# Kernel tuning notes

Hardware: AMD Instinct MI355X
Metric: run time of the kernel (lower is better)

The kernel has to match this reference:

```python
import jax, jax.numpy as jnp
import numpy as np

N_PATHS = 100000
N_STEPS = 512          # number of Euler steps; paths have N_STEPS+1 time points
DT = 0.004             # step_size (~1/250, daily)
KAPPA = 1.0
THETA = 0.04
SIGMA = 0.2
RHO = -0.7
S0 = 100.0
V0 = 0.04


def setup_inputs() -> dict:
    key = jax.random.key(0)
    z = jax.random.normal(key, (N_PATHS, N_STEPS, 2), dtype=jnp.float32)
    return {"z": z}


def reference(z):
    # Euler-Maruyama simulation of the Heston SDE with full-truncation clamp:
    #   dS = S * sqrt(v) dW1
    #   dv = kappa*(theta - v) dt + sigma*sqrt(v) dW2,  corr(dW1,dW2)=rho
    sqdt = jnp.sqrt(jnp.float32(DT))
    c = jnp.sqrt(jnp.float32(1.0 - RHO * RHO))

    def step(carry, zt):
        s, v = carry                      # each [N]
        vp = jnp.maximum(v, 0.0)
        sv = jnp.sqrt(vp)
        dW1 = sqdt * zt[:, 0]
        dW2 = RHO * dW1 + c * sqdt * zt[:, 1]
        s_new = s + s * sv * dW1
        v_new = jnp.maximum(v + KAPPA * (THETA - vp) * DT + SIGMA * sv * dW2, 0.0)
        return (s_new, v_new), (s_new, v_new)

    s0 = jnp.full((N_PATHS,), S0, dtype=z.dtype)
    v0 = jnp.full((N_PATHS,), V0, dtype=z.dtype)
    _, (ss, vs) = jax.lax.scan(step, (s0, v0), jnp.transpose(z, (1, 0, 2)))

    prices = jnp.concatenate([s0[None], ss], axis=0).T      # [N, T+1]
    variances = jnp.concatenate([v0[None], vs], axis=0).T   # [N, T+1]

    # variance-swap price: cumsum of variance * dt + analytic remaining leg L
    tau = jnp.linspace(N_STEPS * DT, 0.0, N_STEPS + 1).astype(z.dtype)  # [T+1]
    L = (variances - THETA) / KAPPA * (1.0 - jnp.exp(-KAPPA * tau)) + THETA * tau
    varswap = jnp.cumsum(variances, axis=1) * DT + L        # [N, T+1]

    # [N, T+1, 3] = (price, variance, varswap price)
    return jnp.stack([prices, variances, varswap], axis=-1)
```

## Files before the change

kernel.cpp:

```cpp
#include <hip/hip_runtime.h>
#include <hip/hip_fp16.h>


#define N_PATHS 100000
#define N_STEPS 512
#define TROW    1539
#define PPB     48
#define BT      128
#define SUB     16
#define NSUB    32
#define U32ROW  770
#define DTc     0.004f
#define EDT     1.0040080107f

typedef float  f32x4  __attribute__((ext_vector_type(4)));
typedef __fp16 fp16x2 __attribute__((ext_vector_type(2)));

__device__ __forceinline__ unsigned pk2(float a, float b) {
    union { fp16x2 h; unsigned u; } cv;
    cv.h = __builtin_amdgcn_cvt_pkrtz(a, b);
    return cv.u;
}
__device__ __forceinline__ float exlo(unsigned w) {
    return __half2float(__ushort_as_half((unsigned short)(w & 0xFFFFu)));
}
__device__ __forceinline__ float exhi(unsigned w) {
    return __half2float(__ushort_as_half((unsigned short)(w >> 16)));
}

__global__ __launch_bounds__(BT)
void heston_kernel(const float* __restrict__ z, float* __restrict__ out) {
    __shared__ unsigned L32[PPB * U32ROW];

    const int tid = threadIdx.x;
    const int p0  = blockIdx.x * PPB;
    const int lim = (N_PATHS - p0 < PPB) ? (N_PATHS - p0) : PPB;

    if (tid < 64) {
        const int  lp  = tid;
        const bool act = (lp < PPB) && (p0 + lp < N_PATHS);
        const int  pc  = (p0 + lp < N_PATHS) ? (p0 + lp) : (N_PATHS - 1);
        const char* zp = (const char*)z + (size_t)pc * 4096;

        f32x4 fA[8], fB[8], fC[8];
        #pragma unroll
        for (int j = 0; j < 8; ++j) fA[j] = *(const f32x4*)(zp + 16 * j);
        #pragma unroll
        for (int j = 0; j < 8; ++j) fB[j] = *(const f32x4*)(zp + 128 + 16 * j);

        float s = 100.0f, v = 0.04f, acc = 0.04f, tau = 2.048f, e = expf(-2.048f);
        float sP = 0.f, vP = 0.f, vsP = 0.f;

        auto doSub = [&](int sc, f32x4 (&cur)[8], f32x4 (&pre)[8]) {
            if (sc + 2 < NSUB) {
                const char* zc = zp + (size_t)(sc + 2) * 128;
                #pragma unroll
                for (int j = 0; j < 8; ++j) pre[j] = *(const f32x4*)(zc + 16 * j);
            }
            const int ub = lp * U32ROW + sc * 24;
            #pragma unroll
            for (int dt = 0; dt < SUB; ++dt) {
                const f32x4 q  = cur[dt >> 1];
                const float z0 = (dt & 1) ? q.z : q.x;
                const float z1 = (dt & 1) ? q.w : q.y;

                const float vp  = fmaxf(v, 0.0f);
                const float sv  = __builtin_amdgcn_sqrtf(vp);
                const float dW1 = 0.06324555320f * z0;
                const float dW2 = fmaf(-0.7f, dW1, 0.04516636050f * z1);
                s = fmaf(s * sv, dW1, s);
                v = fmaxf(fmaf(0.2f * sv, dW2, fmaf(0.04f - vp, DTc, v)), 0.0f);
                acc += v;
                tau -= DTc;
                e *= EDT;
                const float vs = fmaf(acc, DTc, fmaf(0.04f, tau, (v - 0.04f) * (1.0f - e)));

                if (dt & 1) {
                    if (act) {
                        const int d = ub + 3 * (dt >> 1);
                        L32[d + 0] = pk2(sP, vP);
                        L32[d + 1] = pk2(vsP, s);
                        L32[d + 2] = pk2(v, vs);
                    }
                } else { sP = s; vP = v; vsP = vs; }
            }
        };

        for (int g = 0; g < 30; g += 3) {
            doSub(g + 0, fA, fC);
            doSub(g + 1, fB, fA);
            doSub(g + 2, fC, fB);
        }
        doSub(30, fA, fC);
        doSub(31, fB, fA);
    }

    __syncthreads();

    const int wv = tid >> 6;
    const int j  = tid & 63;

    for (int r = wv; r < lim; r += 2) {
        const size_t R0 = (size_t)(p0 + r) * TROW;
        float* gr = out + R0;
        const int hb = r * U32ROW;

        if (j < 3) gr[j] = (j == 0) ? 100.0f : ((j == 1) ? 0.04f : 0.08208f);

        const int lead = (int)((0u - (unsigned)((R0 + 3) & 3u)) & 3u);
        const int ng   = (1536 - lead) >> 2;
        const int tl   = (1536 - lead) & 3;

        if (j < lead) {
            const unsigned w = L32[hb + (j >> 1)];
            gr[3 + j] = (j & 1) ? exhi(w) : exlo(w);
        }
        if (j < tl) {
            const int idx = lead + 4 * ng + j;
            const unsigned w = L32[hb + (idx >> 1)];
            gr[3 + idx] = (idx & 1) ? exhi(w) : exlo(w);
        }

        const int sh = (lead & 1) * 16;
        float* gbase = gr + 3 + lead;
        #pragma unroll
        for (int k = 0; k < 6; ++k) {
            const int g = j + 64 * k;
            if (g < ng) {
                const int idx = lead + 4 * g;
                const int w0  = hb + (idx >> 1);
                const unsigned W0 = L32[w0];
                const unsigned W1 = L32[w0 + 1];
                const unsigned W2 = L32[w0 + 2];
                const unsigned lo = __builtin_amdgcn_alignbit(W1, W0, sh);
                const unsigned hi = __builtin_amdgcn_alignbit(W2, W1, sh);
                f32x4 o;
                o.x = exlo(lo); o.y = exhi(lo);
                o.z = exlo(hi); o.w = exhi(hi);
                *(f32x4*)(gbase + 4 * g) = o;
            }
        }
    }
}

extern "C" void kernel_launch(void* const* d_in, const int* in_sizes, int n_in,
                              void* d_out, int out_size, void* d_ws, size_t ws_size,
                              hipStream_t stream) {
    const float* z = (const float*)d_in[0];
    float* out = (float*)d_out;
    const int nblocks = (N_PATHS + PPB - 1) / PPB;
    heston_kernel<<<nblocks, BT, 0, stream>>>(z, out);
}
```

Baseline: 356.2 us.

## Make blocks persistent and double-buffer LDS so simulation overlaps output writes

Turns the kernel into a persistent grid of 256 blocks, each handling 17 tiles of 24 paths. Wave 0 simulates tile t into one half of a double-buffered LDS area while waves 1 and 2 expand and write tile t-1 from the other half to global memory. The goal is to hide the serial simulation latency behind the output stores instead of running the two phases back to back in each block. The trade-offs are fewer paths per simulating wave (24 of 64 lanes active), a per-tile barrier, and only 256 blocks to fill the GPU.

Result: slower. 473.8 us (+33.0%).

```diff
diff --git a/kernel.cpp b/kernel.cpp
--- a/kernel.cpp
+++ b/kernel.cpp
@@ -5,11 +5,13 @@
 #define N_PATHS 100000
 #define N_STEPS 512
 #define TROW    1539
-#define PPB     48
-#define BT      128
+#define PPB     24
+#define TTILES  17
+#define BT      192
 #define SUB     16
 #define NSUB    32
 #define U32ROW  770
+#define BUFU    (PPB * U32ROW)
 #define DTc     0.004f
 #define EDT     1.0040080107f
 
@@ -30,17 +32,20 @@
 
 __global__ __launch_bounds__(BT)
 void heston_kernel(const float* __restrict__ z, float* __restrict__ out) {
-    __shared__ unsigned L32[PPB * U32ROW];
+    __shared__ unsigned L32[2 * BUFU];
 
     const int tid = threadIdx.x;
-    const int p0  = blockIdx.x * PPB;
-    const int lim = (N_PATHS - p0 < PPB) ? (N_PATHS - p0) : PPB;
+    const int wv  = tid >> 6;
+    const int ln  = tid & 63;
+    const size_t pbase0 = (size_t)blockIdx.x * (PPB * TTILES);
 
-    if (tid < 64) {
-        const int  lp  = tid;
-        const bool act = (lp < PPB) && (p0 + lp < N_PATHS);
-        const int  pc  = (p0 + lp < N_PATHS) ? (p0 + lp) : (N_PATHS - 1);
-        const char* zp = (const char*)z + (size_t)pc * 4096;
+    auto simTile = [&](int t) {
+        const size_t pb = pbase0 + (size_t)t * PPB;
+        if (pb >= N_PATHS) return;
+        unsigned* buf = &L32[(t & 1) * BUFU];
+        const bool act = (ln < PPB) && (pb + ln < N_PATHS);
+        const size_t pc = (pb + ln < N_PATHS) ? (pb + ln) : (N_PATHS - 1);
+        const char* zp = (const char*)z + pc * 4096;
 
         f32x4 fA[8], fB[8], fC[8];
         #pragma unroll
@@ -57,7 +62,7 @@
                 #pragma unroll
                 for (int j = 0; j < 8; ++j) pre[j] = *(const f32x4*)(zc + 16 * j);
             }
-            const int ub = lp * U32ROW + sc * 24;
+            const int ub = ln * U32ROW + sc * 24;
             #pragma unroll
             for (int dt = 0; dt < SUB; ++dt) {
                 const f32x4 q  = cur[dt >> 1];
@@ -78,9 +83,9 @@
                 if (dt & 1) {
                     if (act) {
                         const int d = ub + 3 * (dt >> 1);
-                        L32[d + 0] = pk2(sP, vP);
-                        L32[d + 1] = pk2(vsP, s);
-                        L32[d + 2] = pk2(v, vs);
+                        buf[d + 0] = pk2(sP, vP);
+                        buf[d + 1] = pk2(vsP, s);
+                        buf[d + 2] = pk2(v, vs);
                     }
                 } else { sP = s; vP = v; vsP = vs; }
             }
@@ -93,54 +98,66 @@
         }
         doSub(30, fA, fC);
         doSub(31, fB, fA);
-    }
+    };
 
-    __syncthreads();
+    auto expTile = [&](int t) {
+        const size_t pb = pbase0 + (size_t)t * PPB;
+        if (pb >= N_PATHS) return;
+        const int lim = (int)((N_PATHS - pb < PPB) ? (N_PATHS - pb) : PPB);
+        const unsigned* buf = &L32[(t & 1) * BUFU];
+        const int j = ln;
 
-    const int wv = tid >> 6;
-    const int j  = tid & 63;
+        for (int rr = 0; rr < 12; ++rr) {
+            const int r = (wv - 1) * 12 + rr;
+            if (r >= lim) break;
+            const size_t R0 = (pb + r) * (size_t)TROW;
+            float* gr = out + R0;
+            const int hb = r * U32ROW;
 
-    for (int r = wv; r < lim; r += 2) {
-        const size_t R0 = (size_t)(p0 + r) * TROW;
-        float* gr = out + R0;
-        const int hb = r * U32ROW;
+            if (j < 3) gr[j] = (j == 0) ? 100.0f : ((j == 1) ? 0.04f : 0.08208f);
 
-        if (j < 3) gr[j] = (j == 0) ? 100.0f : ((j == 1) ? 0.04f : 0.08208f);
+            const int lead = (int)((0u - (unsigned)((R0 + 3) & 3u)) & 3u);
+            const int ng   = (1536 - lead) >> 2;
+            const int tl   = (1536 - lead) & 3;
 
-        const int lead = (int)((0u - (unsigned)((R0 + 3) & 3u)) & 3u);
-        const int ng   = (1536 - lead) >> 2;
-        const int tl   = (1536 - lead) & 3;
+            if (j < lead) {
+                const unsigned w = buf[hb + (j >> 1)];
+                gr[3 + j] = (j & 1) ? exhi(w) : exlo(w);
+            }
+            if (j < tl) {
+                const int idx = lead + 4 * ng + j;
+                const unsigned w = buf[hb + (idx >> 1)];
+                gr[3 + idx] = (idx & 1) ? exhi(w) : exlo(w);
+            }
 
-        if (j < lead) {
-            const unsigned w = L32[hb + (j >> 1)];
-            gr[3 + j] = (j & 1) ? exhi(w) : exlo(w);
-        }
-        if (j < tl) {
-            const int idx = lead + 4 * ng + j;
-            const unsigned w = L32[hb + (idx >> 1)];
-            gr[3 + idx] = (idx & 1) ? exhi(w) : exlo(w);
-        }
-
-        const int sh = (lead & 1) * 16;
-        float* gbase = gr + 3 + lead;
-        #pragma unroll
-        for (int k = 0; k < 6; ++k) {
-            const int g = j + 64 * k;
-            if (g < ng) {
-                const int idx = lead + 4 * g;
-                const int w0  = hb + (idx >> 1);
-                const unsigned W0 = L32[w0];
-                const unsigned W1 = L32[w0 + 1];
-                const unsigned W2 = L32[w0 + 2];
-                const unsigned lo = __builtin_amdgcn_alignbit(W1, W0, sh);
-                const unsigned hi = __builtin_amdgcn_alignbit(W2, W1, sh);
-                f32x4 o;
-                o.x = exlo(lo); o.y = exhi(lo);
-                o.z = exlo(hi); o.w = exhi(hi);
-                *(f32x4*)(gbase + 4 * g) = o;
+            const int sh = (lead & 1) * 16;
+            float* gbase = gr + 3 + lead;
+            #pragma unroll
+            for (int k = 0; k < 6; ++k) {
+                const int g = j + 64 * k;
+                if (g < ng) {
+                    const int idx = lead + 4 * g;
+                    const int w0  = hb + (idx >> 1);
+                    const unsigned W0 = buf[w0];
+                    const unsigned W1 = buf[w0 + 1];
+                    const unsigned W2 = buf[w0 + 2];
+                    const unsigned lo = __builtin_amdgcn_alignbit(W1, W0, sh);
+                    const unsigned hi = __builtin_amdgcn_alignbit(W2, W1, sh);
+                    f32x4 o;
+                    o.x = exlo(lo); o.y = exhi(lo);
+                    o.z = exlo(hi); o.w = exhi(hi);
+                    *(f32x4*)(gbase + 4 * g) = o;
+                }
             }
         }
+    };
+
+    for (int t = 0; t < TTILES; ++t) {
+        if (wv == 0)      simTile(t);
+        else if (t >= 1)  expTile(t - 1);
+        __syncthreads();
     }
+    if (wv > 0) expTile(TTILES - 1);
 }
 
 extern "C" void kernel_launch(void* const* d_in, const int* in_sizes, int n_in,
@@ -148,6 +165,5 @@
                               hipStream_t stream) {
     const float* z = (const float*)d_in[0];
     float* out = (float*)d_out;
-    const int nblocks = (N_PATHS + PPB - 1) / PPB;
-    heston_kernel<<<nblocks, BT, 0, stream>>>(z, out);
+    heston_kernel<<<256, BT, 0, stream>>>(z, out);
 }
```

## Warp-specialize into loader, compute and writer waves with double-buffered LDS

Applied to the files above, without the earlier changes.

Restructures the kernel into a persistent 256-block grid where each block handles 392 paths in groups of 40, split into four time-quarters. Wave 0 stages z through LDS, wave 1 runs the Heston recurrence from LDS and packs fp16 results, and wave 2 expands and writes output, all pipelined through double buffers with a barrier per slot. The aim is to overlap global loads, the serial recurrence and the stores instead of running them in sequential phases. In exchange only 40 lanes do compute, every slot needs a block-wide barrier, and 256 blocks may underfill the device.

Measured after the change: 504.4 us. 41.6% more time.

```diff
diff --git a/kernel.cpp b/kernel.cpp
--- a/kernel.cpp
+++ b/kernel.cpp
@@ -5,11 +5,11 @@
 #define N_PATHS 100000
 #define N_STEPS 512
 #define TROW    1539
-#define PPB     48
-#define BT      128
-#define SUB     16
-#define NSUB    32
-#define U32ROW  770
+#define PPG     40
+#define GPB     392
+#define BT      192
+#define ZWRD    260
+#define OWRD    194
 #define DTc     0.004f
 #define EDT     1.0040080107f
 
@@ -30,116 +30,117 @@
 
 __global__ __launch_bounds__(BT)
 void heston_kernel(const float* __restrict__ z, float* __restrict__ out) {
-    __shared__ unsigned L32[PPB * U32ROW];
+    __shared__ float    zb[2][PPG * ZWRD];
+    __shared__ unsigned ob[2][PPG * OWRD];
 
     const int tid = threadIdx.x;
-    const int p0  = blockIdx.x * PPB;
-    const int lim = (N_PATHS - p0 < PPB) ? (N_PATHS - p0) : PPB;
+    const int wv  = tid >> 6;
+    const int ln  = tid & 63;
+    const size_t pbase = (size_t)blockIdx.x * GPB;
+    if (pbase >= N_PATHS) return;
+    const int npath = (int)((N_PATHS - pbase < GPB) ? (N_PATHS - pbase) : GPB);
+    const int ngrp  = (npath + PPG - 1) / PPG;
+    const int nslot = ngrp * 4;
 
-    if (tid < 64) {
-        const int  lp  = tid;
-        const bool act = (lp < PPB) && (p0 + lp < N_PATHS);
-        const int  pc  = (p0 + lp < N_PATHS) ? (p0 + lp) : (N_PATHS - 1);
-        const char* zp = (const char*)z + (size_t)pc * 4096;
+    float s = 0.f, v = 0.f, acc = 0.f, tau = 0.f, e = 0.f;
+    const float E0 = expf(-2.048f);
 
-        f32x4 fA[8], fB[8], fC[8];
-        #pragma unroll
-        for (int j = 0; j < 8; ++j) fA[j] = *(const f32x4*)(zp + 16 * j);
-        #pragma unroll
-        for (int j = 0; j < 8; ++j) fB[j] = *(const f32x4*)(zp + 128 + 16 * j);
-
-        float s = 100.0f, v = 0.04f, acc = 0.04f, tau = 2.048f, e = expf(-2.048f);
-        float sP = 0.f, vP = 0.f, vsP = 0.f;
-
-        auto doSub = [&](int sc, f32x4 (&cur)[8], f32x4 (&pre)[8]) {
-            if (sc + 2 < NSUB) {
-                const char* zc = zp + (size_t)(sc + 2) * 128;
-                #pragma unroll
-                for (int j = 0; j < 8; ++j) pre[j] = *(const f32x4*)(zc + 16 * j);
+    for (int slot = 0; slot < nslot + 2; ++slot) {
+        if (wv == 0 && slot < nslot) {
+            const int g = slot >> 2, q = slot & 3;
+            float* dst = zb[slot & 1];
+            const size_t prow = pbase + (size_t)g * PPG;
+            #pragma unroll 4
+            for (int r = 0; r < PPG; ++r) {
+                size_t pr = prow + r; if (pr > N_PATHS - 1) pr = N_PATHS - 1;
+                const f32x4 d = *(const f32x4*)((const char*)z + pr * 4096 + q * 1024 + ln * 16);
+                *(f32x4*)&dst[r * ZWRD + 4 * ln] = d;
             }
-            const int ub = lp * U32ROW + sc * 24;
-            #pragma unroll
-            for (int dt = 0; dt < SUB; ++dt) {
-                const f32x4 q  = cur[dt >> 1];
-                const float z0 = (dt & 1) ? q.z : q.x;
-                const float z1 = (dt & 1) ? q.w : q.y;
-
-                const float vp  = fmaxf(v, 0.0f);
-                const float sv  = __builtin_amdgcn_sqrtf(vp);
-                const float dW1 = 0.06324555320f * z0;
-                const float dW2 = fmaf(-0.7f, dW1, 0.04516636050f * z1);
-                s = fmaf(s * sv, dW1, s);
-                v = fmaxf(fmaf(0.2f * sv, dW2, fmaf(0.04f - vp, DTc, v)), 0.0f);
-                acc += v;
-                tau -= DTc;
-                e *= EDT;
-                const float vs = fmaf(acc, DTc, fmaf(0.04f, tau, (v - 0.04f) * (1.0f - e)));
-
-                if (dt & 1) {
-                    if (act) {
-                        const int d = ub + 3 * (dt >> 1);
-                        L32[d + 0] = pk2(sP, vP);
-                        L32[d + 1] = pk2(vsP, s);
-                        L32[d + 2] = pk2(v, vs);
-                    }
-                } else { sP = s; vP = v; vsP = vs; }
-            }
-        };
-
-        for (int g = 0; g < 30; g += 3) {
-            doSub(g + 0, fA, fC);
-            doSub(g + 1, fB, fA);
-            doSub(g + 2, fC, fB);
-        }
-        doSub(30, fA, fC);
-        doSub(31, fB, fA);
-    }
-
-    __syncthreads();
-
-    const int wv = tid >> 6;
-    const int j  = tid & 63;
-
-    for (int r = wv; r < lim; r += 2) {
-        const size_t R0 = (size_t)(p0 + r) * TROW;
-        float* gr = out + R0;
-        const int hb = r * U32ROW;
-
-        if (j < 3) gr[j] = (j == 0) ? 100.0f : ((j == 1) ? 0.04f : 0.08208f);
-
-        const int lead = (int)((0u - (unsigned)((R0 + 3) & 3u)) & 3u);
-        const int ng   = (1536 - lead) >> 2;
-        const int tl   = (1536 - lead) & 3;
-
-        if (j < lead) {
-            const unsigned w = L32[hb + (j >> 1)];
-            gr[3 + j] = (j & 1) ? exhi(w) : exlo(w);
-        }
-        if (j < tl) {
-            const int idx = lead + 4 * ng + j;
-            const unsigned w = L32[hb + (idx >> 1)];
-            gr[3 + idx] = (idx & 1) ? exhi(w) : exlo(w);
         }
 
-        const int sh = (lead & 1) * 16;
-        float* gbase = gr + 3 + lead;
-        #pragma unroll
-        for (int k = 0; k < 6; ++k) {
-            const int g = j + 64 * k;
-            if (g < ng) {
-                const int idx = lead + 4 * g;
-                const int w0  = hb + (idx >> 1);
-                const unsigned W0 = L32[w0];
-                const unsigned W1 = L32[w0 + 1];
-                const unsigned W2 = L32[w0 + 2];
-                const unsigned lo = __builtin_amdgcn_alignbit(W1, W0, sh);
-                const unsigned hi = __builtin_amdgcn_alignbit(W2, W1, sh);
-                f32x4 o;
-                o.x = exlo(lo); o.y = exhi(lo);
-                o.z = exlo(hi); o.w = exhi(hi);
-                *(f32x4*)(gbase + 4 * g) = o;
+        if (wv == 1 && slot >= 1 && slot <= nslot) {
+            const int s1 = slot - 1, q = s1 & 3;
+            if (ln < PPG) {
+                const float* src = zb[s1 & 1] + ln * ZWRD;
+                unsigned*    dst = ob[s1 & 1] + ln * OWRD;
+                if (q == 0) { s = 100.0f; v = 0.04f; acc = 0.04f; tau = 2.048f; e = E0; }
+                float sP = 0.f, vP = 0.f, vsP = 0.f;
+                #pragma unroll 8
+                for (int d2 = 0; d2 < 64; ++d2) {
+                    const f32x4 qz = *(const f32x4*)&src[4 * d2];
+                    #pragma unroll
+                    for (int half = 0; half < 2; ++half) {
+                        const float z0 = half ? qz.z : qz.x;
+                        const float z1 = half ? qz.w : qz.y;
+                        const float vp  = fmaxf(v, 0.0f);
+                        const float sv  = __builtin_amdgcn_sqrtf(vp);
+                        const float dW1 = 0.06324555320f * z0;
+                        const float dW2 = fmaf(-0.7f, dW1, 0.04516636050f * z1);
+                        s = fmaf(s * sv, dW1, s);
+                        v = fmaxf(fmaf(0.2f * sv, dW2, fmaf(0.04f - vp, DTc, v)), 0.0f);
+                        acc += v;
+                        tau -= DTc;
+                        e *= EDT;
+                        const float vs = fmaf(acc, DTc, fmaf(0.04f, tau, (v - 0.04f) * (1.0f - e)));
+                        if (half) {
+                            dst[3 * d2 + 0] = pk2(sP, vP);
+                            dst[3 * d2 + 1] = pk2(vsP, s);
+                            dst[3 * d2 + 2] = pk2(v, vs);
+                        } else { sP = s; vP = v; vsP = vs; }
+                    }
+                }
             }
         }
+
+        if (wv == 2 && slot >= 2) {
+            const int s2 = slot - 2, g = s2 >> 2, q = s2 & 3;
+            const unsigned* buf = ob[s2 & 1];
+            const int j = ln;
+            for (int r = 0; r < PPG; ++r) {
+                const size_t prow = pbase + (size_t)g * PPG + r;
+                const unsigned* lr = buf + r * OWRD;
+                float* gr = out + prow * (size_t)TROW;
+
+                if (q == 0 && j < 3)
+                    gr[j] = (j == 0) ? 100.0f : ((j == 1) ? 0.04f : 0.08208f);
+
+                const size_t base = prow * (size_t)TROW + 3 + 384 * q;
+                float* gq = gr + 3 + 384 * q;
+                const int lead = (int)((0u - (unsigned)(base & 3u)) & 3u);
+                const int ng   = (384 - lead) >> 2;
+                const int tl   = (384 - lead) & 3;
+
+                if (j < lead) {
+                    const unsigned w = lr[j >> 1];
+                    gq[j] = (j & 1) ? exhi(w) : exlo(w);
+                }
+                if (j < tl) {
+                    const int idx = lead + 4 * ng + j;
+                    const unsigned w = lr[idx >> 1];
+                    gq[idx] = (idx & 1) ? exhi(w) : exlo(w);
+                }
+                const int sh = (lead & 1) * 16;
+                #pragma unroll
+                for (int k = 0; k < 2; ++k) {
+                    const int gI = j + 64 * k;
+                    if (gI < ng) {
+                        const int idx = lead + 4 * gI;
+                        const int w0  = idx >> 1;
+                        const unsigned W0 = lr[w0];
+                        const unsigned W1 = lr[w0 + 1];
+                        const unsigned W2 = lr[w0 + 2];
+                        const unsigned lo = __builtin_amdgcn_alignbit(W1, W0, sh);
+                        const unsigned hi = __builtin_amdgcn_alignbit(W2, W1, sh);
+                        f32x4 o;
+                        o.x = exlo(lo); o.y = exhi(lo);
+                        o.z = exlo(hi); o.w = exhi(hi);
+                        *(f32x4*)(gq + lead + 4 * gI) = o;
+                    }
+                }
+            }
+        }
+
+        __syncthreads();
     }
 }
 
@@ -148,6 +149,5 @@
                               hipStream_t stream) {
     const float* z = (const float*)d_in[0];
     float* out = (float*)d_out;
-    const int nblocks = (N_PATHS + PPB - 1) / PPB;
-    heston_kernel<<<nblocks, BT, 0, stream>>>(z, out);
+    heston_kernel<<<256, BT, 0, stream>>>(z, out);
 }
```
